# Kernel optimization log

Measured on AMD Instinct MI355X. Metric: run time of the kernel, lower is better.

Reference implementation:

```python
import jax, jax.numpy as jnp
from jax import lax
import numpy as np

ARG_NAMES = ('x w1 b1 bn1_g bn1_b bn1_m bn1_v w2 b2 bn2_g bn2_b bn2_m bn2_v w3 b3 w4 b4 '
             'attn_w attn_b attn_u g0_w1 g0_b1 g0_w2 g0_b2 g1_w1 g1_b1 g1_w2 g1_b2 '
             'g2_w1 g2_b1 g2_w2 g2_b2 c_w1 c_b1 c_w2 c_b2 c_w3 c_b3 c_w4 c_b4').split()


def _conv1d(x, w, b, stride, pad):
    # x: [N, C, L], w: [O, I, K]
    y = lax.conv_general_dilated(x, w, (stride,), [(pad, pad)],
                                 dimension_numbers=('NCH', 'OIH', 'NCH'))
    return y + b[None, :, None]


def _bn(x, g, b, m, v, eps=1e-5):
    # eval-mode BatchNorm1d over channel dim of [N, C, L]
    inv = g / jnp.sqrt(v + eps)
    return (x - m[None, :, None]) * inv[None, :, None] + b[None, :, None]


def _forward(x, w1, b1, bn1_g, bn1_b, bn1_m, bn1_v, w2, b2, bn2_g, bn2_b, bn2_m, bn2_v,
             w3, b3, w4, b4, attn_w, attn_b, attn_u,
             g0_w1, g0_b1, g0_w2, g0_b2, g1_w1, g1_b1, g1_w2, g1_b2,
             g2_w1, g2_b1, g2_w2, g2_b2,
             c_w1, c_b1, c_w2, c_b2, c_w3, c_b3, c_w4, c_b4):
    B, S, C, T = x.shape  # [batch, crops, channels=64, time=400]
    h = x.reshape(-1, C, T)
    # CNN stack (dropout = identity in eval)
    h = _bn(jax.nn.elu(_conv1d(h, w1, b1, 2, 1)), bn1_g, bn1_b, bn1_m, bn1_v)   # [N,64,192]
    h = _bn(jax.nn.elu(_conv1d(h, w2, b2, 2, 0)), bn2_g, bn2_b, bn2_m, bn2_v)   # [N,64,87]
    h = jax.nn.elu(_conv1d(h, w3, b3, 1, 0))                                    # [N,64,82]
    h = lax.reduce_window(h, 0.0, lax.add, (1, 1, 3), (1, 1, 2), 'VALID') / 3.0  # [N,64,40]
    h = jax.nn.elu(_conv1d(h, w4, b4, 1, 0))                                    # [N,64,35]
    h = h.reshape(B, S, C, -1)  # [B, S, 64, 35]
    # Attention pooling over the crop dim (dim=1), sum=True
    v = jnp.tanh(jnp.einsum('bsch,hd->bscd', h, attn_w) + attn_b)
    alphas = jax.nn.softmax(jnp.einsum('bscd,d->bsc', v, attn_u), axis=1)
    h = jax.nn.elu((h * alphas[..., None]).sum(axis=1))  # [B, 64, 35]
    # GIN over complete 64-node graph (self-loops included, eps=0):
    # aggregation per node == sum over all nodes of the graph
    def gin(h, W1, B1, W2, B2):
        agg = h + h.sum(axis=1, keepdims=True)
        return jax.nn.relu(agg @ W1 + B1) @ W2 + B2
    h = jax.nn.relu(gin(h, g0_w1, g0_b1, g0_w2, g0_b2))
    h = jax.nn.relu(gin(h, g1_w1, g1_b1, g1_w2, g1_b2))
    h = gin(h, g2_w1, g2_b1, g2_w2, g2_b2)  # no act after last layer
    # Classifier
    f = h.reshape(B, -1)  # [B, 2240]
    f = jax.nn.elu(f @ c_w1 + c_b1)
    f = jax.nn.elu(f @ c_w2 + c_b2)
    f = jax.nn.elu(f @ c_w3 + c_b3)
    return f @ c_w4 + c_b4  # [B, 2]


def setup_inputs() -> dict:
    key = jax.random.key(0)
    ks = iter(jax.random.split(key, 64))
    def rn(shape, s=0.05):
        return jax.random.normal(next(ks), shape, dtype=jnp.float32) * s
    d = {}
    d['x'] = jax.random.normal(next(ks), (32, 16, 64, 400), dtype=jnp.float32)
    d['w1'] = rn((64, 64, 20)); d['b1'] = rn((64,))
    d['bn1_g'] = jnp.ones((64,), jnp.float32); d['bn1_b'] = jnp.zeros((64,), jnp.float32)
    d['bn1_m'] = jnp.zeros((64,), jnp.float32); d['bn1_v'] = jnp.ones((64,), jnp.float32)
    d['w2'] = rn((64, 64, 20)); d['b2'] = rn((64,))
    d['bn2_g'] = jnp.ones((64,), jnp.float32); d['bn2_b'] = jnp.zeros((64,), jnp.float32)
    d['bn2_m'] = jnp.zeros((64,), jnp.float32); d['bn2_v'] = jnp.ones((64,), jnp.float32)
    d['w3'] = rn((64, 64, 6)); d['b3'] = rn((64,))
    d['w4'] = rn((64, 64, 6)); d['b4'] = rn((64,))
    d['attn_w'] = rn((35, 256), 0.1); d['attn_b'] = rn((256,), 0.1); d['attn_u'] = rn((256,), 0.1)
    d['g0_w1'] = rn((35, 256)); d['g0_b1'] = rn((256,))
    d['g0_w2'] = rn((256, 256)); d['g0_b2'] = rn((256,))
    d['g1_w1'] = rn((256, 256)); d['g1_b1'] = rn((256,))
    d['g1_w2'] = rn((256, 256)); d['g1_b2'] = rn((256,))
    d['g2_w1'] = rn((256, 35)); d['g2_b1'] = rn((35,))
    d['g2_w2'] = rn((35, 35)); d['g2_b2'] = rn((35,))
    d['c_w1'] = rn((2240, 256)); d['c_b1'] = rn((256,))
    d['c_w2'] = rn((256, 64)); d['c_b2'] = rn((64,))
    d['c_w3'] = rn((64, 16)); d['c_b3'] = rn((16,))
    d['c_w4'] = rn((16, 2)); d['c_b4'] = rn((2,))
    return d


def reference(x, w1, b1, bn1_g, bn1_b, bn1_m, bn1_v, w2, b2, bn2_g, bn2_b, bn2_m, bn2_v,
              w3, b3, w4, b4, attn_w, attn_b, attn_u,
              g0_w1, g0_b1, g0_w2, g0_b2, g1_w1, g1_b1, g1_w2, g1_b2,
              g2_w1, g2_b1, g2_w2, g2_b2,
              c_w1, c_b1, c_w2, c_b2, c_w3, c_b3, c_w4, c_b4):
    return _forward(x, w1, b1, bn1_g, bn1_b, bn1_m, bn1_v, w2, b2, bn2_g, bn2_b, bn2_m, bn2_v,
                    w3, b3, w4, b4, attn_w, attn_b, attn_u,
                    g0_w1, g0_b1, g0_w2, g0_b2, g1_w1, g1_b1, g1_w2, g1_b2,
                    g2_w1, g2_b1, g2_w2, g2_b2,
                    c_w1, c_b1, c_w2, c_b2, c_w3, c_b3, c_w4, c_b4)
```

## Files before the change

### kernel.cpp

```cpp
#include <hip/hip_runtime.h>
#include <math.h>

typedef __attribute__((ext_vector_type(8))) __bf16 bf16x8;
typedef __attribute__((ext_vector_type(4))) float f32x4;

__device__ __forceinline__ float elu_f(float v) {
    return v > 0.f ? v : (expf(v) - 1.f);
}

__global__ __launch_bounds__(256) void prep_weights(
    const float* __restrict__ w1, const float* __restrict__ w2,
    const float* __restrict__ w3, const float* __restrict__ w4,
    __bf16* __restrict__ t1, __bf16* __restrict__ t2,
    __bf16* __restrict__ t3, __bf16* __restrict__ t4)
{
    int idx = blockIdx.x * 256 + threadIdx.x;
    if (idx < 81920) {
        int k = idx / 4096, r = idx - k * 4096, co = r >> 6, ci = r & 63;
        t1[idx] = (__bf16)w1[(co * 64 + ci) * 20 + k];
    } else if (idx < 163840) {
        int j = idx - 81920;
        int k = j / 4096, r = j - k * 4096, co = r >> 6, ci = r & 63;
        t2[j] = (__bf16)w2[(co * 64 + ci) * 20 + k];
    } else if (idx < 188416) {
        int j = idx - 163840;
        int k = j / 4096, r = j - k * 4096, co = r >> 6, ci = r & 63;
        t3[j] = (__bf16)w3[(co * 64 + ci) * 6 + k];
    } else if (idx < 212992) {
        int j = idx - 188416;
        int k = j / 4096, r = j - k * 4096, co = r >> 6, ci = r & 63;
        t4[j] = (__bf16)w4[(co * 64 + ci) * 6 + k];
    }
}

__global__ __launch_bounds__(256) void prep_tr(
    const float* __restrict__ g0w1, const float* __restrict__ g0w2,
    const float* __restrict__ g1w1, const float* __restrict__ g1w2,
    const float* __restrict__ g2w1, const float* __restrict__ g2w2,
    __bf16* __restrict__ d0, __bf16* __restrict__ d1, __bf16* __restrict__ d2,
    __bf16* __restrict__ d3, __bf16* __restrict__ d4, __bf16* __restrict__ d5)
{
    int bid = blockIdx.x;
    const float* src; __bf16* dst; int K, O, Kpad, Opad, tile;
    if (bid < 4)       { src = g0w1; dst = d0; K = 35;   O = 256; Kpad = 64;   Opad = 256; tile = bid; }
    else if (bid < 20) { src = g0w2; dst = d1; K = 256;  O = 256; Kpad = 256;  Opad = 256; tile = bid - 4; }
    else if (bid < 36) { src = g1w1; dst = d2; K = 256;  O = 256; Kpad = 256;  Opad = 256; tile = bid - 20; }
    else if (bid < 52) { src = g1w2; dst = d3; K = 256;  O = 256; Kpad = 256;  Opad = 256; tile = bid - 36; }
    else if (bid < 56) { src = g2w1; dst = d4; K = 256;  O = 35;  Kpad = 256;  Opad = 64;  tile = bid - 52; }
    else               { src = g2w2; dst = d5; K = 35;   O = 35;  Kpad = 64;   Opad = 64;  tile = 0; }
    int ktiles = Kpad >> 6;
    int ot = tile / ktiles, kt = tile - ot * ktiles;
    int k0 = kt * 64, o0 = ot * 64;
    size_t LOFF = (size_t)Opad * Kpad;
    __shared__ float tl[64][68];
    int c = threadIdx.x & 63, rr = threadIdx.x >> 6;
    #pragma unroll
    for (int it = 0; it < 16; ++it) {
        int r = rr + it * 4;
        int kk = k0 + r, oo = o0 + c;
        tl[r][c] = (kk < K && oo < O) ? src[(size_t)kk * O + oo] : 0.f;
    }
    __syncthreads();
    #pragma unroll
    for (int it = 0; it < 16; ++it) {
        int r = rr + it * 4;
        float v = tl[c][r];
        __bf16 hi = (__bf16)v;
        float lo = v - (float)hi;
        size_t pos = (size_t)(o0 + r) * Kpad + k0 + c;
        dst[pos] = hi;
        dst[LOFF + pos] = (__bf16)lo;
    }
}

template<int K, int STRIDE, int PAD, bool DO_BN, int IMODE,
         int NPB, int TPN, int LIN, int LOUT, int KCHUNK>
__global__ __launch_bounds__(NPB * TPN * 64, 2) void conv_mfma(
    const void* __restrict__ xin, const __bf16* __restrict__ wT,
    const float* __restrict__ bias,
    const float* __restrict__ bn_g, const float* __restrict__ bn_b,
    const float* __restrict__ bn_m, const float* __restrict__ bn_v,
    __bf16* __restrict__ y)
{
    constexpr int THREADS = NPB * TPN * 64;
    constexpr int TBLK  = TPN * 48;
    constexpr int VSPAN = STRIDE * (TBLK - 1) + K;
    constexpr int NBUF  = (STRIDE == 2) ? 2 : 1;
    constexpr int ROWS  = (VSPAN + NBUF - 1) / NBUF;
    __shared__ __align__(16) __bf16 sx[NPB * NBUF * ROWS * 72];
    __shared__ __align__(16) __bf16 sw[KCHUNK * 64 * 72];

    const int tid = threadIdx.x;
    const int nb  = blockIdx.x * NPB;

    if constexpr (IMODE == 0) {
        const float* xg = (const float*)xin + (size_t)nb * 64 * LIN;
        constexpr int NZROWS = PAD + (VSPAN - LIN - PAD);
        if (tid < NZROWS * 64) {
            int zr = tid >> 6;
            int v = (zr < PAD) ? zr : (LIN + PAD + zr - PAD);
            sx[((v & (NBUF - 1)) * ROWS + (v >> (NBUF - 1))) * 72 + (tid & 63)] = (__bf16)0.f;
        }
        constexpr int J4 = LIN / 4;
        constexpr int NCH = 64 * J4;
        constexpr int ITER = NCH / THREADS;
        #pragma unroll
        for (int it = 0; it < ITER; ++it) {
            int idx = it * THREADS + tid;
            int ci = idx / J4, j = idx - ci * J4;
            float4 f = *(const float4*)(xg + (size_t)ci * LIN + 4 * j);
            #pragma unroll
            for (int e = 0; e < 4; ++e) {
                int v = 4 * j + e + PAD;
                sx[((v & (NBUF - 1)) * ROWS + (v >> (NBUF - 1))) * 72 + ci] =
                    (__bf16)((e == 0) ? f.x : (e == 1) ? f.y : (e == 2) ? f.z : f.w);
            }
        }
    } else {
        const __bf16* xg = (const __bf16*)xin;
        constexpr int NSTG = NPB * VSPAN * 8;
        constexpr int ITER = (NSTG + THREADS - 1) / THREADS;
        #pragma unroll
        for (int it = 0; it < ITER; ++it) {
            int idx = it * THREADS + tid;
            if (idx < NSTG) {
                int n_l = idx / (VSPAN * 8);
                int r   = idx - n_l * (VSPAN * 8);
                int v = r >> 3, c8 = (r & 7) * 8;
                int buf = (STRIDE == 2) ? (v & 1) : 0;
                int row = (STRIDE == 2) ? (v >> 1) : v;
                __bf16* dst = sx + ((size_t)(n_l * NBUF + buf) * ROWS + row) * 72 + c8;
                if constexpr (IMODE == 1) {
                    if (v < LIN) {
                        const __bf16* src = xg + (((size_t)(nb + n_l) * LIN + v) * 64 + c8);
                        *(uint4*)dst = *(const uint4*)src;
                    } else {
                        #pragma unroll
                        for (int e = 0; e < 8; ++e) dst[e] = (__bf16)0.f;
                    }
                } else {
                    if (v < LIN) {
                        const __bf16* s0 = xg + (((size_t)(nb + n_l) * 82 + 2 * v) * 64 + c8);
                        #pragma unroll
                        for (int e = 0; e < 8; ++e)
                            dst[e] = (__bf16)(((float)s0[e] + (float)s0[64 + e] +
                                               (float)s0[128 + e]) * (1.f / 3.f));
                    } else {
                        #pragma unroll
                        for (int e = 0; e < 8; ++e) dst[e] = (__bf16)0.f;
                    }
                }
            }
        }
    }

    const int wave = tid >> 6, lane = tid & 63;
    const int n_l  = wave / TPN, tile = wave - n_l * TPN;
    const int m    = lane & 15, quad = lane >> 4;
    const __bf16* sxn = sx + (size_t)n_l * NBUF * ROWS * 72;

    f32x4 acc[3][4];
    #pragma unroll
    for (int mi = 0; mi < 3; ++mi)
        #pragma unroll
        for (int nj = 0; nj < 4; ++nj)
            acc[mi][nj] = (f32x4){0.f, 0.f, 0.f, 0.f};

    for (int kb = 0; kb < K; kb += KCHUNK) {
        if (kb) __syncthreads();
        constexpr int WITER = KCHUNK * 64 * 8 / THREADS;
        #pragma unroll
        for (int it = 0; it < WITER; ++it) {
            int idx = it * THREADS + tid;
            int r = idx >> 3, p = idx & 7;
            *(uint4*)(sw + (size_t)r * 72 + p * 8) =
                *(const uint4*)(wT + (size_t)(kb + (r >> 6)) * 4096 + (r & 63) * 64 + p * 8);
        }
        __syncthreads();

        #pragma unroll
        for (int kp2 = 0; kp2 < KCHUNK; ++kp2) {
            const int kp = kb + kp2;
            const int buf    = (STRIDE == 2) ? (kp & 1) : 0;
            const int rowoff = (STRIDE == 2) ? (kp >> 1) : kp;
            const __bf16* abase = sxn + ((size_t)buf * ROWS + tile * 48 + m + rowoff) * 72;
            const __bf16* bbase = sw + (size_t)(kp2 * 64 + m) * 72;
            #pragma unroll
            for (int s = 0; s < 2; ++s) {
                bf16x8 af[3], bfr[4];
                #pragma unroll
                for (int mi = 0; mi < 3; ++mi)
                    af[mi] = *(const bf16x8*)(abase + mi * (16 * 72) + s * 32 + quad * 8);
                #pragma unroll
                for (int nj = 0; nj < 4; ++nj)
                    bfr[nj] = *(const bf16x8*)(bbase + nj * (16 * 72) + s * 32 + quad * 8);
                #pragma unroll
                for (int mi = 0; mi < 3; ++mi)
                    #pragma unroll
                    for (int nj = 0; nj < 4; ++nj)
                        acc[mi][nj] = __builtin_amdgcn_mfma_f32_16x16x32_bf16(
                            af[mi], bfr[nj], acc[mi][nj], 0, 0, 0);
            }
        }
    }

    #pragma unroll
    for (int nj = 0; nj < 4; ++nj) {
        const int co = nj * 16 + m;
        const float bi = bias[co];
        float scale = 1.f, shift = 0.f;
        if constexpr (DO_BN) {
            float inv = bn_g[co] / sqrtf(bn_v[co] + 1e-5f);
            scale = inv; shift = bn_b[co] - bn_m[co] * inv;
        }
        #pragma unroll
        for (int mi = 0; mi < 3; ++mi) {
            #pragma unroll
            for (int r = 0; r < 4; ++r) {
                int t = tile * 48 + mi * 16 + quad * 4 + r;
                if (t < LOUT) {
                    float v = acc[mi][nj][r] + bi;
                    v = elu_f(v);
                    if constexpr (DO_BN) v = v * scale + shift;
                    y[((size_t)(nb + n_l) * LOUT + t) * 64 + co] = (__bf16)v;
                }
            }
        }
    }
}

__global__ __launch_bounds__(256) void attn_pool_k(
    const __bf16* __restrict__ h, const float* __restrict__ W,
    const float* __restrict__ ab, const float* __restrict__ u,
    float* __restrict__ out)
{
    const int b = blockIdx.x >> 6;
    const int c = blockIdx.x & 63;
    __shared__ float sh[16 * 35];
    __shared__ float slog[16];
    __shared__ float sred[4];
    __shared__ float salpha[16];
    const int tid = threadIdx.x;
    for (int idx = tid; idx < 16 * 35; idx += 256) {
        int s = idx / 35, hh = idx - s * 35;
        sh[idx] = (float)h[((size_t)(b * 16 + s) * 35 + hh) * 64 + c];
    }
    __syncthreads();
    float Wc[35];
    #pragma unroll
    for (int k = 0; k < 35; ++k) Wc[k] = W[k * 256 + tid];
    const float myb = ab[tid], myu = u[tid];
    for (int s = 0; s < 16; ++s) {
        float dot = myb;
        #pragma unroll
        for (int k = 0; k < 35; ++k) dot = fmaf(sh[s * 35 + k], Wc[k], dot);
        float val = tanhf(dot) * myu;
        #pragma unroll
        for (int off = 32; off > 0; off >>= 1) val += __shfl_down(val, off, 64);
        if ((tid & 63) == 0) sred[tid >> 6] = val;
        __syncthreads();
        if (tid == 0) slog[s] = sred[0] + sred[1] + sred[2] + sred[3];
        __syncthreads();
    }
    if (tid == 0) {
        float mx = slog[0];
        for (int s = 1; s < 16; ++s) mx = fmaxf(mx, slog[s]);
        float sum = 0.f, e[16];
        for (int s = 0; s < 16; ++s) { e[s] = expf(slog[s] - mx); sum += e[s]; }
        float inv = 1.f / sum;
        for (int s = 0; s < 16; ++s) salpha[s] = e[s] * inv;
    }
    __syncthreads();
    if (tid < 35) {
        float acc = 0.f;
        for (int s = 0; s < 16; ++s) acc = fmaf(sh[s * 35 + tid], salpha[s], acc);
        out[((size_t)(b * 64 + c)) * 35 + tid] = elu_f(acc);
    }
}

#define APLANE (64 * 264)

__device__ __forceinline__ void gin_gemm_dev(
    const __bf16* As,
    const __bf16* __restrict__ Wg, int Kpad, int wlo, int Kout,
    const float* __restrict__ bias,
    int mode,
    __bf16* Ad, float* __restrict__ outg)
{
    const int lane = threadIdx.x & 63;
    const int wave_o0 = (threadIdx.x >> 6) * 64;
    if (wave_o0 >= ((Kout + 63) & ~63)) return;
    const int m = lane & 15, quad = lane >> 4;

    f32x4 acc[4][4];
    #pragma unroll
    for (int mi = 0; mi < 4; ++mi)
        #pragma unroll
        for (int nj = 0; nj < 4; ++nj)
            acc[mi][nj] = (f32x4){0.f, 0.f, 0.f, 0.f};

    for (int k0 = 0; k0 < Kpad; k0 += 32) {
        bf16x8 ah[4], al[4], bh[4], bl[4];
        #pragma unroll
        for (int mi = 0; mi < 4; ++mi) {
            const __bf16* ap = As + (size_t)(mi * 16 + m) * 264 + k0 + quad * 8;
            ah[mi] = *(const bf16x8*)ap;
            al[mi] = *(const bf16x8*)(ap + APLANE);
        }
        #pragma unroll
        for (int nj = 0; nj < 4; ++nj) {
            const __bf16* wp = Wg + (size_t)(wave_o0 + nj * 16 + m) * Kpad + k0 + quad * 8;
            bh[nj] = *(const bf16x8*)wp;
            bl[nj] = *(const bf16x8*)(wp + wlo);
        }
        #pragma unroll
        for (int mi = 0; mi < 4; ++mi)
            #pragma unroll
            for (int nj = 0; nj < 4; ++nj) {
                acc[mi][nj] = __builtin_amdgcn_mfma_f32_16x16x32_bf16(
                    al[mi], bh[nj], acc[mi][nj], 0, 0, 0);
                acc[mi][nj] = __builtin_amdgcn_mfma_f32_16x16x32_bf16(
                    ah[mi], bl[nj], acc[mi][nj], 0, 0, 0);
                acc[mi][nj] = __builtin_amdgcn_mfma_f32_16x16x32_bf16(
                    ah[mi], bh[nj], acc[mi][nj], 0, 0, 0);
            }
    }

    #pragma unroll
    for (int nj = 0; nj < 4; ++nj) {
        const int o = wave_o0 + nj * 16 + m;
        const bool ovalid = (o < Kout);
        const float bi = ovalid ? bias[o] : 0.f;
        float v[4][4];
        #pragma unroll
        for (int mi = 0; mi < 4; ++mi)
            #pragma unroll
            for (int r = 0; r < 4; ++r)
                v[mi][r] = acc[mi][nj][r] + bi;
        if (mode == 2) {
            if (ovalid) {
                #pragma unroll
                for (int mi = 0; mi < 4; ++mi)
                    #pragma unroll
                    for (int r = 0; r < 4; ++r)
                        outg[(size_t)(mi * 16 + quad * 4 + r) * Kout + o] = v[mi][r];
            }
        } else {
            float s = 0.f;
            #pragma unroll
            for (int mi = 0; mi < 4; ++mi)
                #pragma unroll
                for (int r = 0; r < 4; ++r) {
                    float rv = ovalid ? fmaxf(v[mi][r], 0.f) : 0.f;
                    v[mi][r] = rv;
                    s += rv;
                }
            if (mode == 1) {
                s += __shfl_xor(s, 16, 64);
                s += __shfl_xor(s, 32, 64);
            } else {
                s = 0.f;
            }
            #pragma unroll
            for (int mi = 0; mi < 4; ++mi)
                #pragma unroll
                for (int r = 0; r < 4; ++r) {
                    float a = v[mi][r] + s;
                    __bf16 hi = (__bf16)a;
                    size_t pos = (size_t)(mi * 16 + quad * 4 + r) * 264 + o;
                    Ad[pos] = hi;
                    Ad[APLANE + pos] = (__bf16)(a - (float)hi);
                }
        }
    }
}

__global__ __launch_bounds__(256) void gin_fused(
    const float* __restrict__ ha,
    const __bf16* __restrict__ gW0a, const __bf16* __restrict__ gW0b,
    const __bf16* __restrict__ gW1a, const __bf16* __restrict__ gW1b,
    const __bf16* __restrict__ gW2a, const __bf16* __restrict__ gW2b,
    const float* __restrict__ b0a, const float* __restrict__ b0b,
    const float* __restrict__ b1a, const float* __restrict__ b1b,
    const float* __restrict__ b2a, const float* __restrict__ b2b,
    float* __restrict__ H3)
{
    const int b = blockIdx.x, tid = threadIdx.x;
    __shared__ __align__(16) __bf16 sA[2][2 * APLANE];
    __shared__ float sS[64];
    const float* hab = ha + (size_t)b * 2240;

    if (tid < 64) {
        float s = 0.f;
        if (tid < 35)
            for (int n = 0; n < 64; ++n) s += hab[n * 35 + tid];
        sS[tid] = s;
    }
    __syncthreads();
    for (int idx = tid; idx < 64 * 64; idx += 256) {
        int n = idx >> 6, k = idx & 63;
        float a = (k < 35) ? hab[n * 35 + k] + sS[k] : 0.f;
        __bf16 hi = (__bf16)a;
        sA[0][n * 264 + k] = hi;
        sA[0][APLANE + n * 264 + k] = (__bf16)(a - (float)hi);
    }
    __syncthreads();

    gin_gemm_dev(sA[0], gW0a, 64,  16384, 256, b0a, 0, sA[1], nullptr); __syncthreads();
    gin_gemm_dev(sA[1], gW0b, 256, 65536, 256, b0b, 1, sA[0], nullptr); __syncthreads();
    gin_gemm_dev(sA[0], gW1a, 256, 65536, 256, b1a, 0, sA[1], nullptr); __syncthreads();
    gin_gemm_dev(sA[1], gW1b, 256, 65536, 256, b1b, 1, sA[0], nullptr); __syncthreads();
    gin_gemm_dev(sA[0], gW2a, 256, 16384, 35,  b2a, 0, sA[1], nullptr); __syncthreads();
    gin_gemm_dev(sA[1], gW2b, 64,  4096,  35,  b2b, 2, nullptr, H3 + (size_t)b * 2240);
}

__global__ __launch_bounds__(256) void cls1_part_k(
    const float* __restrict__ H3, const float* __restrict__ w1,
    float* __restrict__ s1p)
{
    const int b  = blockIdx.x;
    const int kc = blockIdx.y;
    const int k0 = kc * 140;
    __shared__ float sH[140];
    const int tid = threadIdx.x;
    if (tid < 140) sH[tid] = H3[(size_t)b * 2240 + k0 + tid];
    __syncthreads();
    const int o = (tid >> 6) * 64 + (tid & 63);
    float a0 = 0.f, a1 = 0.f, a2 = 0.f, a3 = 0.f;
    const float* wr = w1 + (size_t)k0 * 256 + o;
    #pragma unroll
    for (int k = 0; k < 140; k += 4) {
        a0 = fmaf(sH[k],     wr[(size_t)k * 256],       a0);
        a1 = fmaf(sH[k + 1], wr[(size_t)(k + 1) * 256], a1);
        a2 = fmaf(sH[k + 2], wr[(size_t)(k + 2) * 256], a2);
        a3 = fmaf(sH[k + 3], wr[(size_t)(k + 3) * 256], a3);
    }
    s1p[((size_t)kc * 32 + b) * 256 + o] = a0 + a1 + a2 + a3;
}

__global__ __launch_bounds__(256) void cls234_k(
    const float* __restrict__ s1p, const float* __restrict__ b1,
    const float* __restrict__ w2, const float* __restrict__ b2,
    const float* __restrict__ w3, const float* __restrict__ b3,
    const float* __restrict__ w4, const float* __restrict__ b4,
    float* __restrict__ out)
{
    const int b = blockIdx.x, tid = threadIdx.x;
    __shared__ float s1[256];
    __shared__ float part[4][64];
    __shared__ float s2[64];
    __shared__ float s3[16];
    {
        float acc = b1[tid];
        #pragma unroll
        for (int kc = 0; kc < 16; ++kc)
            acc += s1p[((size_t)kc * 32 + b) * 256 + tid];
        s1[tid] = elu_f(acc);
    }
    __syncthreads();
    {
        int kg = tid >> 6, o = tid & 63;
        float acc = 0.f;
        for (int k = kg * 64; k < kg * 64 + 64; ++k)
            acc = fmaf(s1[k], w2[k * 64 + o], acc);
        part[kg][o] = acc;
    }
    __syncthreads();
    if (tid < 64) {
        float acc = part[0][tid] + part[1][tid] + part[2][tid] + part[3][tid] + b2[tid];
        s2[tid] = elu_f(acc);
    }
    __syncthreads();
    if (tid < 16) {
        float acc = b3[tid];
        for (int k = 0; k < 64; ++k) acc = fmaf(s2[k], w3[k * 16 + tid], acc);
        s3[tid] = elu_f(acc);
    }
    __syncthreads();
    if (tid < 2) {
        float acc = b4[tid];
        for (int k = 0; k < 16; ++k) acc = fmaf(s3[k], w4[k * 2 + tid], acc);
        out[b * 2 + tid] = acc;
    }
}

extern "C" void kernel_launch(void* const* d_in, const int* in_sizes, int n_in,
                              void* d_out, int out_size, void* d_ws, size_t ws_size,
                              hipStream_t stream)
{
    const float* x     = (const float*)d_in[0];
    const float* w1    = (const float*)d_in[1];
    const float* b1    = (const float*)d_in[2];
    const float* bn1_g = (const float*)d_in[3];
    const float* bn1_b = (const float*)d_in[4];
    const float* bn1_m = (const float*)d_in[5];
    const float* bn1_v = (const float*)d_in[6];
    const float* w2    = (const float*)d_in[7];
    const float* b2    = (const float*)d_in[8];
    const float* bn2_g = (const float*)d_in[9];
    const float* bn2_b = (const float*)d_in[10];
    const float* bn2_m = (const float*)d_in[11];
    const float* bn2_v = (const float*)d_in[12];
    const float* w3    = (const float*)d_in[13];
    const float* b3    = (const float*)d_in[14];
    const float* w4    = (const float*)d_in[15];
    const float* b4    = (const float*)d_in[16];
    const float* attn_w = (const float*)d_in[17];
    const float* attn_b = (const float*)d_in[18];
    const float* attn_u = (const float*)d_in[19];
    const float* g0_w1 = (const float*)d_in[20];
    const float* g0_b1 = (const float*)d_in[21];
    const float* g0_w2 = (const float*)d_in[22];
    const float* g0_b2 = (const float*)d_in[23];
    const float* g1_w1 = (const float*)d_in[24];
    const float* g1_b1 = (const float*)d_in[25];
    const float* g1_w2 = (const float*)d_in[26];
    const float* g1_b2 = (const float*)d_in[27];
    const float* g2_w1 = (const float*)d_in[28];
    const float* g2_b1 = (const float*)d_in[29];
    const float* g2_w2 = (const float*)d_in[30];
    const float* g2_b2 = (const float*)d_in[31];
    const float* c_w1  = (const float*)d_in[32];
    const float* c_b1  = (const float*)d_in[33];
    const float* c_w2  = (const float*)d_in[34];
    const float* c_b2  = (const float*)d_in[35];
    const float* c_w3  = (const float*)d_in[36];
    const float* c_b3  = (const float*)d_in[37];
    const float* c_w4  = (const float*)d_in[38];
    const float* c_b4  = (const float*)d_in[39];
    float* out = (float*)d_out;

    char* ws = (char*)d_ws;
    __bf16* wT1  = (__bf16*)(ws + 0);
    __bf16* wT2  = (__bf16*)(ws + 163840);
    __bf16* wT3  = (__bf16*)(ws + 327680);
    __bf16* wT4  = (__bf16*)(ws + 376832);
    __bf16* h1   = (__bf16*)(ws + 425984);
    __bf16* h2   = (__bf16*)(ws + 13008896);
    __bf16* h3   = (__bf16*)(ws + 18710528);
    __bf16* h4   = (__bf16*)(ws + 24084480);
    float*  ha   = (float*)(ws + 26378240);
    __bf16* gW0a = (__bf16*)(ws + 26664960);
    __bf16* gW0b = (__bf16*)(ws + 26730496);
    __bf16* gW1a = (__bf16*)(ws + 26992640);
    __bf16* gW1b = (__bf16*)(ws + 27254784);
    __bf16* gW2a = (__bf16*)(ws + 27516928);
    __bf16* gW2b = (__bf16*)(ws + 27582464);
    float*  H3   = (float*)(ws + 27598848);
    float*  s1p  = (float*)(ws + 27885568);

    prep_weights<<<dim3(832), dim3(256), 0, stream>>>(w1, w2, w3, w4, wT1, wT2, wT3, wT4);
    prep_tr<<<dim3(57), dim3(256), 0, stream>>>(g0_w1, g0_w2, g1_w1, g1_w2, g2_w1, g2_w2,
                                                gW0a, gW0b, gW1a, gW1b, gW2a, gW2b);

    conv_mfma<20, 2, 1, true, 0, 1, 4, 400, 192, 2><<<dim3(512), dim3(256), 0, stream>>>(
        x, wT1, b1, bn1_g, bn1_b, bn1_m, bn1_v, h1);
    conv_mfma<20, 2, 0, true, 1, 1, 2, 192, 87, 2><<<dim3(512), dim3(128), 0, stream>>>(
        h1, wT2, b2, bn2_g, bn2_b, bn2_m, bn2_v, h2);
    conv_mfma<6, 1, 0, false, 1, 1, 2, 87, 82, 2><<<dim3(512), dim3(128), 0, stream>>>(
        h2, wT3, b3, nullptr, nullptr, nullptr, nullptr, h3);
    conv_mfma<6, 1, 0, false, 2, 2, 1, 40, 35, 2><<<dim3(256), dim3(128), 0, stream>>>(
        h3, wT4, b4, nullptr, nullptr, nullptr, nullptr, h4);

    attn_pool_k<<<dim3(2048), dim3(256), 0, stream>>>(h4, attn_w, attn_b, attn_u, ha);

    gin_fused<<<dim3(32), dim3(256), 0, stream>>>(
        ha, gW0a, gW0b, gW1a, gW1b, gW2a, gW2b,
        g0_b1, g0_b2, g1_b1, g1_b2, g2_b1, g2_b2, H3);

    cls1_part_k<<<dim3(32, 16), dim3(256), 0, stream>>>(H3, c_w1, s1p);
    cls234_k<<<dim3(32), dim3(256), 0, stream>>>(s1p, c_b1, c_w2, c_b2, c_w3, c_b3,
                                                 c_w4, c_b4, out);
}
```

Measured before the change: 339.3 us.

## Stream conv weights directly into registers and widen GIN kernel to 8 waves

The conv kernels no longer stage weight slices in shared memory behind block barriers. Each lane now loads its B-fragments straight from global memory into a double-buffered register set, prefetching the next tap while the current one runs through MFMA. Separately, the fused GIN kernel is launched with 512 threads and each wave covers 32 output columns instead of 64, doubling the waves per block. This trades LDS traffic and syncs for more global/L2 loads and register pressure, and gives the serial GIN stage more parallelism per block.

```diff
diff --git a/kernel.cpp b/kernel.cpp
--- a/kernel.cpp
+++ b/kernel.cpp
@@ -74,7 +74,7 @@
 }
 
 template<int K, int STRIDE, int PAD, bool DO_BN, int IMODE,
-         int NPB, int TPN, int LIN, int LOUT, int KCHUNK>
+         int NPB, int TPN, int LIN, int LOUT>
 __global__ __launch_bounds__(NPB * TPN * 64, 2) void conv_mfma(
     const void* __restrict__ xin, const __bf16* __restrict__ wT,
     const float* __restrict__ bias,
@@ -88,7 +88,6 @@
     constexpr int NBUF  = (STRIDE == 2) ? 2 : 1;
     constexpr int ROWS  = (VSPAN + NBUF - 1) / NBUF;
     __shared__ __align__(16) __bf16 sx[NPB * NBUF * ROWS * 72];
-    __shared__ __align__(16) __bf16 sw[KCHUNK * 64 * 72];
 
     const int tid = threadIdx.x;
     const int nb  = blockIdx.x * NPB;
@@ -153,6 +152,7 @@
             }
         }
     }
+    __syncthreads();
 
     const int wave = tid >> 6, lane = tid & 63;
     const int n_l  = wave / TPN, tile = wave - n_l * TPN;
@@ -166,41 +166,40 @@
         for (int nj = 0; nj < 4; ++nj)
             acc[mi][nj] = (f32x4){0.f, 0.f, 0.f, 0.f};
 
-    for (int kb = 0; kb < K; kb += KCHUNK) {
-        if (kb) __syncthreads();
-        constexpr int WITER = KCHUNK * 64 * 8 / THREADS;
-        #pragma unroll
-        for (int it = 0; it < WITER; ++it) {
-            int idx = it * THREADS + tid;
-            int r = idx >> 3, p = idx & 7;
-            *(uint4*)(sw + (size_t)r * 72 + p * 8) =
-                *(const uint4*)(wT + (size_t)(kb + (r >> 6)) * 4096 + (r & 63) * 64 + p * 8);
-        }
-        __syncthreads();
-
-        #pragma unroll
-        for (int kp2 = 0; kp2 < KCHUNK; ++kp2) {
-            const int kp = kb + kp2;
-            const int buf    = (STRIDE == 2) ? (kp & 1) : 0;
-            const int rowoff = (STRIDE == 2) ? (kp >> 1) : kp;
-            const __bf16* abase = sxn + ((size_t)buf * ROWS + tile * 48 + m + rowoff) * 72;
-            const __bf16* bbase = sw + (size_t)(kp2 * 64 + m) * 72;
-            #pragma unroll
-            for (int s = 0; s < 2; ++s) {
-                bf16x8 af[3], bfr[4];
+    const __bf16* wlane = wT + (size_t)m * 64 + quad * 8;
+    bf16x8 wreg[2][8];
+    #pragma unroll
+    for (int nj = 0; nj < 4; ++nj)
+        #pragma unroll
+        for (int s = 0; s < 2; ++s)
+            wreg[0][nj * 2 + s] = *(const bf16x8*)(wlane + nj * 1024 + s * 32);
+
+    #pragma unroll
+    for (int kp = 0; kp < K; ++kp) {
+        const int cur = kp & 1, nxt = cur ^ 1;
+        if (kp + 1 < K) {
+            const __bf16* wnext = wlane + (size_t)(kp + 1) * 4096;
+            #pragma unroll
+            for (int nj = 0; nj < 4; ++nj)
                 #pragma unroll
-                for (int mi = 0; mi < 3; ++mi)
-                    af[mi] = *(const bf16x8*)(abase + mi * (16 * 72) + s * 32 + quad * 8);
+                for (int s = 0; s < 2; ++s)
+                    wreg[nxt][nj * 2 + s] = *(const bf16x8*)(wnext + nj * 1024 + s * 32);
+        }
+        const int buf    = (STRIDE == 2) ? (kp & 1) : 0;
+        const int rowoff = (STRIDE == 2) ? (kp >> 1) : kp;
+        const __bf16* abase = sxn + ((size_t)buf * ROWS + tile * 48 + m + rowoff) * 72;
+        #pragma unroll
+        for (int s = 0; s < 2; ++s) {
+            bf16x8 af[3];
+            #pragma unroll
+            for (int mi = 0; mi < 3; ++mi)
+                af[mi] = *(const bf16x8*)(abase + mi * (16 * 72) + s * 32 + quad * 8);
+            #pragma unroll
+            for (int mi = 0; mi < 3; ++mi)
                 #pragma unroll
                 for (int nj = 0; nj < 4; ++nj)
-                    bfr[nj] = *(const bf16x8*)(bbase + nj * (16 * 72) + s * 32 + quad * 8);
-                #pragma unroll
-                for (int mi = 0; mi < 3; ++mi)
-                    #pragma unroll
-                    for (int nj = 0; nj < 4; ++nj)
-                        acc[mi][nj] = __builtin_amdgcn_mfma_f32_16x16x32_bf16(
-                            af[mi], bfr[nj], acc[mi][nj], 0, 0, 0);
-            }
+                    acc[mi][nj] = __builtin_amdgcn_mfma_f32_16x16x32_bf16(
+                        af[mi], wreg[cur][nj * 2 + s], acc[mi][nj], 0, 0, 0);
         }
     }
 
@@ -288,19 +287,20 @@
     __bf16* Ad, float* __restrict__ outg)
 {
     const int lane = threadIdx.x & 63;
-    const int wave_o0 = (threadIdx.x >> 6) * 64;
-    if (wave_o0 >= ((Kout + 63) & ~63)) return;
+    const int wave = threadIdx.x >> 6;
+    const int o0 = wave * 32;
+    if (o0 >= ((Kout + 63) & ~63)) return;
     const int m = lane & 15, quad = lane >> 4;
 
-    f32x4 acc[4][4];
+    f32x4 acc[4][2];
     #pragma unroll
     for (int mi = 0; mi < 4; ++mi)
         #pragma unroll
-        for (int nj = 0; nj < 4; ++nj)
+        for (int nj = 0; nj < 2; ++nj)
             acc[mi][nj] = (f32x4){0.f, 0.f, 0.f, 0.f};
 
     for (int k0 = 0; k0 < Kpad; k0 += 32) {
-        bf16x8 ah[4], al[4], bh[4], bl[4];
+        bf16x8 ah[4], al[4], bh[2], bl[2];
         #pragma unroll
         for (int mi = 0; mi < 4; ++mi) {
             const __bf16* ap = As + (size_t)(mi * 16 + m) * 264 + k0 + quad * 8;
@@ -308,15 +308,15 @@
             al[mi] = *(const bf16x8*)(ap + APLANE);
         }
         #pragma unroll
-        for (int nj = 0; nj < 4; ++nj) {
-            const __bf16* wp = Wg + (size_t)(wave_o0 + nj * 16 + m) * Kpad + k0 + quad * 8;
+        for (int nj = 0; nj < 2; ++nj) {
+            const __bf16* wp = Wg + (size_t)(o0 + nj * 16 + m) * Kpad + k0 + quad * 8;
             bh[nj] = *(const bf16x8*)wp;
             bl[nj] = *(const bf16x8*)(wp + wlo);
         }
         #pragma unroll
         for (int mi = 0; mi < 4; ++mi)
             #pragma unroll
-            for (int nj = 0; nj < 4; ++nj) {
+            for (int nj = 0; nj < 2; ++nj) {
                 acc[mi][nj] = __builtin_amdgcn_mfma_f32_16x16x32_bf16(
                     al[mi], bh[nj], acc[mi][nj], 0, 0, 0);
                 acc[mi][nj] = __builtin_amdgcn_mfma_f32_16x16x32_bf16(
@@ -327,8 +327,8 @@
     }
 
     #pragma unroll
-    for (int nj = 0; nj < 4; ++nj) {
-        const int o = wave_o0 + nj * 16 + m;
+    for (int nj = 0; nj < 2; ++nj) {
+        const int o = o0 + nj * 16 + m;
         const bool ovalid = (o < Kout);
         const float bi = ovalid ? bias[o] : 0.f;
         float v[4][4];
@@ -375,7 +375,7 @@
     }
 }
 
-__global__ __launch_bounds__(256) void gin_fused(
+__global__ __launch_bounds__(512) void gin_fused(
     const float* __restrict__ ha,
     const __bf16* __restrict__ gW0a, const __bf16* __restrict__ gW0b,
     const __bf16* __restrict__ gW1a, const __bf16* __restrict__ gW1b,
@@ -397,7 +397,7 @@
         sS[tid] = s;
     }
     __syncthreads();
-    for (int idx = tid; idx < 64 * 64; idx += 256) {
+    for (int idx = tid; idx < 64 * 64; idx += 512) {
         int n = idx >> 6, k = idx & 63;
         float a = (k < 35) ? hab[n * 35 + k] + sS[k] : 0.f;
         __bf16 hi = (__bf16)a;
@@ -553,18 +553,18 @@
     prep_tr<<<dim3(57), dim3(256), 0, stream>>>(g0_w1, g0_w2, g1_w1, g1_w2, g2_w1, g2_w2,
                                                 gW0a, gW0b, gW1a, gW1b, gW2a, gW2b);
 
-    conv_mfma<20, 2, 1, true, 0, 1, 4, 400, 192, 2><<<dim3(512), dim3(256), 0, stream>>>(
+    conv_mfma<20, 2, 1, true, 0, 1, 4, 400, 192><<<dim3(512), dim3(256), 0, stream>>>(
         x, wT1, b1, bn1_g, bn1_b, bn1_m, bn1_v, h1);
-    conv_mfma<20, 2, 0, true, 1, 1, 2, 192, 87, 2><<<dim3(512), dim3(128), 0, stream>>>(
+    conv_mfma<20, 2, 0, true, 1, 1, 2, 192, 87><<<dim3(512), dim3(128), 0, stream>>>(
         h1, wT2, b2, bn2_g, bn2_b, bn2_m, bn2_v, h2);
-    conv_mfma<6, 1, 0, false, 1, 1, 2, 87, 82, 2><<<dim3(512), dim3(128), 0, stream>>>(
+    conv_mfma<6, 1, 0, false, 1, 1, 2, 87, 82><<<dim3(512), dim3(128), 0, stream>>>(
         h2, wT3, b3, nullptr, nullptr, nullptr, nullptr, h3);
-    conv_mfma<6, 1, 0, false, 2, 2, 1, 40, 35, 2><<<dim3(256), dim3(128), 0, stream>>>(
+    conv_mfma<6, 1, 0, false, 2, 2, 1, 40, 35><<<dim3(256), dim3(128), 0, stream>>>(
         h3, wT4, b4, nullptr, nullptr, nullptr, nullptr, h4);
 
     attn_pool_k<<<dim3(2048), dim3(256), 0, stream>>>(h4, attn_w, attn_b, attn_u, ha);
 
-    gin_fused<<<dim3(32), dim3(256), 0, stream>>>(
+    gin_fused<<<dim3(32), dim3(512), 0, stream>>>(
         ha, gW0a, gW0b, gW1a, gW1b, gW2a, gW2b,
         g0_b1, g0_b2, g1_b1, g1_b2, g2_b1, g2_b2, H3);
 
```

Result: slower. 363.2 us (+7.0%).

## Restructure attention pooling per wave and widen GIN blocks to 512 threads

Applied to the files above, without the earlier changes.

The attention pooling kernel now handles four (batch, channel) pairs per block, one wave each. The attention weights are staged once in shared memory, and each lane computes scores for 16 crops times 4 hidden units, then reduces them with wave shuffles. This removes the per-crop block-wide barriers and the single-thread softmax. The GIN kernel now launches 512 threads, and each wave takes a 32-column output tile instead of 64, doubling the waves available on only 32 blocks. The costs are higher register pressure in the pooling kernel and a 35 KB weight load into shared memory per block.

```diff
diff --git a/kernel.cpp b/kernel.cpp
--- a/kernel.cpp
+++ b/kernel.cpp
@@ -234,47 +234,71 @@
     const float* __restrict__ ab, const float* __restrict__ u,
     float* __restrict__ out)
 {
-    const int b = blockIdx.x >> 6;
-    const int c = blockIdx.x & 63;
-    __shared__ float sh[16 * 35];
-    __shared__ float slog[16];
-    __shared__ float sred[4];
-    __shared__ float salpha[16];
+    __shared__ float sW[35 * 256];
+    __shared__ float sh[4][16 * 35 + 5];
     const int tid = threadIdx.x;
-    for (int idx = tid; idx < 16 * 35; idx += 256) {
-        int s = idx / 35, hh = idx - s * 35;
-        sh[idx] = (float)h[((size_t)(b * 16 + s) * 35 + hh) * 64 + c];
-    }
-    __syncthreads();
-    float Wc[35];
-    #pragma unroll
-    for (int k = 0; k < 35; ++k) Wc[k] = W[k * 256 + tid];
-    const float myb = ab[tid], myu = u[tid];
+    const int pair0 = blockIdx.x * 4;
+    for (int i = tid; i < 35 * 256; i += 256) sW[i] = W[i];
+    for (int i = tid; i < 4 * 560; i += 256) {
+        int q = i / 560, r = i - q * 560;
+        int s = r / 35, t = r - s * 35;
+        int bc = pair0 + q, b = bc >> 6, c = bc & 63;
+        sh[q][s * 35 + t] = (float)h[(((size_t)b * 16 + s) * 35 + t) * 64 + c];
+    }
+    __syncthreads();
+
+    const int wave = tid >> 6, lane = tid & 63;
+    const int bc = pair0 + wave;
+    const float* shw = sh[wave];
+
+    float myu[4], myb[4];
+    #pragma unroll
+    for (int p = 0; p < 4; ++p) { myu[p] = u[lane + 64 * p]; myb[p] = ab[lane + 64 * p]; }
+
+    float dot[16][4];
+    #pragma unroll
+    for (int s = 0; s < 16; ++s)
+        #pragma unroll
+        for (int p = 0; p < 4; ++p) dot[s][p] = myb[p];
+
+    for (int t = 0; t < 35; ++t) {
+        float w0 = sW[t * 256 + lane];
+        float w1 = sW[t * 256 + lane + 64];
+        float w2 = sW[t * 256 + lane + 128];
+        float w3 = sW[t * 256 + lane + 192];
+        #pragma unroll
+        for (int s = 0; s < 16; ++s) {
+            float hv = shw[s * 35 + t];
+            dot[s][0] = fmaf(hv, w0, dot[s][0]);
+            dot[s][1] = fmaf(hv, w1, dot[s][1]);
+            dot[s][2] = fmaf(hv, w2, dot[s][2]);
+            dot[s][3] = fmaf(hv, w3, dot[s][3]);
+        }
+    }
+
+    float sc[16];
+    #pragma unroll
     for (int s = 0; s < 16; ++s) {
-        float dot = myb;
-        #pragma unroll
-        for (int k = 0; k < 35; ++k) dot = fmaf(sh[s * 35 + k], Wc[k], dot);
-        float val = tanhf(dot) * myu;
-        #pragma unroll
-        for (int off = 32; off > 0; off >>= 1) val += __shfl_down(val, off, 64);
-        if ((tid & 63) == 0) sred[tid >> 6] = val;
-        __syncthreads();
-        if (tid == 0) slog[s] = sred[0] + sred[1] + sred[2] + sred[3];
-        __syncthreads();
-    }
-    if (tid == 0) {
-        float mx = slog[0];
-        for (int s = 1; s < 16; ++s) mx = fmaxf(mx, slog[s]);
-        float sum = 0.f, e[16];
-        for (int s = 0; s < 16; ++s) { e[s] = expf(slog[s] - mx); sum += e[s]; }
-        float inv = 1.f / sum;
-        for (int s = 0; s < 16; ++s) salpha[s] = e[s] * inv;
-    }
-    __syncthreads();
-    if (tid < 35) {
+        float v = tanhf(dot[s][0]) * myu[0] + tanhf(dot[s][1]) * myu[1]
+                + tanhf(dot[s][2]) * myu[2] + tanhf(dot[s][3]) * myu[3];
+        #pragma unroll
+        for (int off = 1; off < 64; off <<= 1) v += __shfl_xor(v, off, 64);
+        sc[s] = v;
+    }
+
+    float mx = sc[0];
+    #pragma unroll
+    for (int s = 1; s < 16; ++s) mx = fmaxf(mx, sc[s]);
+    float e[16], sum = 0.f;
+    #pragma unroll
+    for (int s = 0; s < 16; ++s) { e[s] = expf(sc[s] - mx); sum += e[s]; }
+    float inv = 1.f / sum;
+
+    if (lane < 35) {
         float acc = 0.f;
-        for (int s = 0; s < 16; ++s) acc = fmaf(sh[s * 35 + tid], salpha[s], acc);
-        out[((size_t)(b * 64 + c)) * 35 + tid] = elu_f(acc);
+        #pragma unroll
+        for (int s = 0; s < 16; ++s) acc = fmaf(shw[s * 35 + lane], e[s] * inv, acc);
+        out[(size_t)bc * 35 + lane] = elu_f(acc);
     }
 }
 
@@ -288,19 +312,20 @@
     __bf16* Ad, float* __restrict__ outg)
 {
     const int lane = threadIdx.x & 63;
-    const int wave_o0 = (threadIdx.x >> 6) * 64;
-    if (wave_o0 >= ((Kout + 63) & ~63)) return;
+    const int wave = threadIdx.x >> 6;
+    const int o0 = wave * 32;
+    if (o0 >= ((Kout + 63) & ~63)) return;
     const int m = lane & 15, quad = lane >> 4;
 
-    f32x4 acc[4][4];
+    f32x4 acc[4][2];
     #pragma unroll
     for (int mi = 0; mi < 4; ++mi)
         #pragma unroll
-        for (int nj = 0; nj < 4; ++nj)
+        for (int nj = 0; nj < 2; ++nj)
             acc[mi][nj] = (f32x4){0.f, 0.f, 0.f, 0.f};
 
     for (int k0 = 0; k0 < Kpad; k0 += 32) {
-        bf16x8 ah[4], al[4], bh[4], bl[4];
+        bf16x8 ah[4], al[4], bh[2], bl[2];
         #pragma unroll
         for (int mi = 0; mi < 4; ++mi) {
             const __bf16* ap = As + (size_t)(mi * 16 + m) * 264 + k0 + quad * 8;
@@ -308,15 +333,15 @@
             al[mi] = *(const bf16x8*)(ap + APLANE);
         }
         #pragma unroll
-        for (int nj = 0; nj < 4; ++nj) {
-            const __bf16* wp = Wg + (size_t)(wave_o0 + nj * 16 + m) * Kpad + k0 + quad * 8;
+        for (int nj = 0; nj < 2; ++nj) {
+            const __bf16* wp = Wg + (size_t)(o0 + nj * 16 + m) * Kpad + k0 + quad * 8;
             bh[nj] = *(const bf16x8*)wp;
             bl[nj] = *(const bf16x8*)(wp + wlo);
         }
         #pragma unroll
         for (int mi = 0; mi < 4; ++mi)
             #pragma unroll
-            for (int nj = 0; nj < 4; ++nj) {
+            for (int nj = 0; nj < 2; ++nj) {
                 acc[mi][nj] = __builtin_amdgcn_mfma_f32_16x16x32_bf16(
                     al[mi], bh[nj], acc[mi][nj], 0, 0, 0);
                 acc[mi][nj] = __builtin_amdgcn_mfma_f32_16x16x32_bf16(
@@ -327,8 +352,8 @@
     }
 
     #pragma unroll
-    for (int nj = 0; nj < 4; ++nj) {
-        const int o = wave_o0 + nj * 16 + m;
+    for (int nj = 0; nj < 2; ++nj) {
+        const int o = o0 + nj * 16 + m;
         const bool ovalid = (o < Kout);
         const float bi = ovalid ? bias[o] : 0.f;
         float v[4][4];
@@ -375,7 +400,7 @@
     }
 }
 
-__global__ __launch_bounds__(256) void gin_fused(
+__global__ __launch_bounds__(512) void gin_fused(
     const float* __restrict__ ha,
     const __bf16* __restrict__ gW0a, const __bf16* __restrict__ gW0b,
     const __bf16* __restrict__ gW1a, const __bf16* __restrict__ gW1b,
@@ -397,7 +422,7 @@
         sS[tid] = s;
     }
     __syncthreads();
-    for (int idx = tid; idx < 64 * 64; idx += 256) {
+    for (int idx = tid; idx < 64 * 64; idx += 512) {
         int n = idx >> 6, k = idx & 63;
         float a = (k < 35) ? hab[n * 35 + k] + sS[k] : 0.f;
         __bf16 hi = (__bf16)a;
@@ -562,9 +587,9 @@
     conv_mfma<6, 1, 0, false, 2, 2, 1, 40, 35, 2><<<dim3(256), dim3(128), 0, stream>>>(
         h3, wT4, b4, nullptr, nullptr, nullptr, nullptr, h4);
 
-    attn_pool_k<<<dim3(2048), dim3(256), 0, stream>>>(h4, attn_w, attn_b, attn_u, ha);
-
-    gin_fused<<<dim3(32), dim3(256), 0, stream>>>(
+    attn_pool_k<<<dim3(512), dim3(256), 0, stream>>>(h4, attn_w, attn_b, attn_u, ha);
+
+    gin_fused<<<dim3(32), dim3(512), 0, stream>>>(
         ha, gW0a, gW0b, gW1a, gW1b, gW2a, gW2b,
         g0_b1, g0_b2, g1_b1, g1_b2, g2_b1, g2_b2, H3);
 
```

Result: faster. 322.7 us (-4.9%).
